# Performance work log

Hardware: AMD Instinct MI355X
Metric: run time of the kernel (lower is better)

## Reference

```python
import jax, jax.numpy as jnp
import numpy as np

B, F_DIM, P, C, H = 16, 256, 8192, 96, 256


def setup_inputs() -> dict:
    key = jax.random.key(0)
    ks = jax.random.split(key, 8)
    seg_feat = jax.random.normal(ks[0], (B, F_DIM, P), dtype=jnp.float32)
    seg_label = jax.random.randint(ks[1], (B, P), 0, C, dtype=jnp.int64 if jax.config.read('jax_enable_x64') else jnp.int32)
    s1 = 1.0 / np.sqrt(F_DIM)
    s2 = 1.0 / np.sqrt(H)
    w1 = jax.random.uniform(ks[2], (F_DIM, H), jnp.float32, -s1, s1)
    b1 = jax.random.uniform(ks[3], (H,), jnp.float32, -s1, s1)
    w2 = jax.random.uniform(ks[4], (H, H), jnp.float32, -s2, s2)
    b2 = jax.random.uniform(ks[5], (H,), jnp.float32, -s2, s2)
    w_logit = jax.random.uniform(ks[6], (H, C), jnp.float32, -s2, s2)
    b_logit = jax.random.uniform(ks[7], (C,), jnp.float32, -s2, s2)
    return dict(seg_feat=seg_feat, seg_label=seg_label, w1=w1, b1=b1,
                w2=w2, b2=b2, w_logit=w_logit, b_logit=b_logit)


def _pool_by_class(seg_feat, seg_label, num_classes):
    # seg_feat: [B, F, P], seg_label: [B, P] -> pooled [B*C, F]
    b, f, p = seg_feat.shape
    seg_ids = (jnp.arange(b, dtype=seg_label.dtype)[:, None] * num_classes
               + seg_label).reshape(-1)                       # [B*P]
    feat = seg_feat.transpose(0, 2, 1).reshape(b * p, f)      # [B*P, F]
    segmax = jax.ops.segment_max(feat, seg_ids, num_segments=b * num_classes)
    counts = jax.ops.segment_sum(jnp.ones((b * p,), feat.dtype), seg_ids,
                                 num_segments=b * num_classes)  # [B*C]
    counts = counts[:, None]
    # torch: max over points of feat * onehot -> zeros from other classes
    # participate in the max unless the class covers ALL points; empty
    # classes pool to 0 (max of all zeros).
    pooled = jnp.where(counts == 0, 0.0,
                       jnp.where(counts == p, segmax, jnp.maximum(segmax, 0.0)))
    return pooled


def reference(seg_feat, seg_label, w1, b1, w2, b2, w_logit, b_logit):
    num_classes = w_logit.shape[1]
    pooled = _pool_by_class(seg_feat, seg_label, num_classes)   # [B*C, F]
    # feat_mlp: Linear+ReLU x2 (dropout_prob=0), then part_logit
    h = jax.nn.relu(pooled @ w1 + b1)
    h = jax.nn.relu(h @ w2 + b2)
    part_pred = h @ w_logit + b_logit                           # [B*C, C]
    b = seg_feat.shape[0]
    part_batch = jnp.repeat(jnp.arange(b), num_classes)
    part_label = jnp.tile(jnp.arange(num_classes), b)
    return part_pred, part_label, part_batch
```

## Files before the change

### kernel.cpp

```cpp
#include <hip/hip_runtime.h>

#define B 16
#define F_DIM 256
#define P 8192
#define C 96
#define H 256
#define NSEG (B * C)
#define G 8
#define NFBLK (F_DIM / G)
#define SPLIT 4
#define PQ (P / SPLIT)


__global__ __launch_bounds__(256) void pool_kernel(const float* __restrict__ feat,
                                                   const int* __restrict__ label,
                                                   int* __restrict__ kbuf,
                                                   int* __restrict__ cnts) {
    __shared__ int smax[G][C];
    __shared__ int hist[C];
    const int blk = blockIdx.x;
    const int q  = blk & 3;
    const int fg = (blk >> 2) & 31;
    const int b  = blk >> 7;
    const int f0 = fg << 3;
    const int t = threadIdx.x;

    for (int i = t; i < G * C; i += 256) ((int*)smax)[i] = 0x80000000;
    if (t < C) hist[t] = 0;
    __syncthreads();

    const int4* lrow4 = (const int4*)(label + (size_t)b * P + (size_t)q * PQ);
    int4 lab[2];
    lab[0] = lrow4[t];
    lab[1] = lrow4[t + 256];

    if (fg == 0) {
        #pragma unroll
        for (int j = 0; j < 2; ++j) {
            atomicAdd(&hist[lab[j].x], 1);
            atomicAdd(&hist[lab[j].y], 1);
            atomicAdd(&hist[lab[j].z], 1);
            atomicAdd(&hist[lab[j].w], 1);
        }
    }

    const float4* fbase4 = (const float4*)(feat + ((size_t)b * F_DIM + f0) * P + (size_t)q * PQ);

    float4 cur[2], nxt[2];
    cur[0] = fbase4[t];
    cur[1] = fbase4[t + 256];

    #pragma unroll
    for (int f = 0; f < G; ++f) {
        if (f + 1 < G) {
            nxt[0] = fbase4[(size_t)(f + 1) * (P / 4) + t];
            nxt[1] = fbase4[(size_t)(f + 1) * (P / 4) + t + 256];
        }
        #pragma unroll
        for (int j = 0; j < 2; ++j) {
            atomicMax(&smax[f][lab[j].x], __float_as_int(cur[j].x));
            atomicMax(&smax[f][lab[j].y], __float_as_int(cur[j].y));
            atomicMax(&smax[f][lab[j].z], __float_as_int(cur[j].z));
            atomicMax(&smax[f][lab[j].w], __float_as_int(cur[j].w));
        }
        cur[0] = nxt[0];
        cur[1] = nxt[1];
    }
    __syncthreads();

    if (fg == 0 && t < C) cnts[q * NSEG + b * C + t] = hist[t];

    if (t < C) {
        int4 lo, hi;
        lo.x = smax[0][t]; lo.y = smax[1][t]; lo.z = smax[2][t]; lo.w = smax[3][t];
        hi.x = smax[4][t]; hi.y = smax[5][t]; hi.z = smax[6][t]; hi.w = smax[7][t];
        int* dst = kbuf + (size_t)q * NSEG * F_DIM + (size_t)(b * C + t) * F_DIM + f0;
        *(int4*)dst = lo;
        *(int4*)(dst + 4) = hi;
    }
}

template <int COLS, int RELU, int OUTW, int POOLIN>
__global__ __launch_bounds__(256, 3) void dense_kernel(const float* __restrict__ x,
                                                       const int* __restrict__ kx,
                                                       const int* __restrict__ cnts,
                                                       const float* __restrict__ w,
                                                       const float* __restrict__ bias,
                                                       float* __restrict__ y,
                                                       float* __restrict__ tails) {
    constexpr int NQ = COLS / 4;
    __shared__ float xs[8][H];
    __shared__ float ps[8][COLS][17];
    const int t = threadIdx.x;
    const int row0 = blockIdx.x * 8;
    const int bj0 = blockIdx.y * COLS;

    if (POOLIN) {
        const int4* k4 = (const int4*)kx;
        const size_t base = (size_t)row0 * (H / 4);
        #pragma unroll
        for (int jj = 0; jj < 2; ++jj) {
            const int i = t + jj * 256;
            int4 km = k4[base + i];
            #pragma unroll
            for (int h = 1; h < SPLIT; ++h) {
                const int4 kh = k4[(size_t)h * NSEG * (H / 4) + base + i];
                km.x = km.x > kh.x ? km.x : kh.x;
                km.y = km.y > kh.y ? km.y : kh.y;
                km.z = km.z > kh.z ? km.z : kh.z;
                km.w = km.w > kh.w ? km.w : kh.w;
            }
            const int row = row0 + (i >> 6);
            const int cnt = cnts[row] + cnts[NSEG + row] +
                            cnts[2 * NSEG + row] + cnts[3 * NSEG + row];
            float4 v;
            v.x = __int_as_float(km.x); v.y = __int_as_float(km.y);
            v.z = __int_as_float(km.z); v.w = __int_as_float(km.w);
            if (cnt == 0) {
                v.x = v.y = v.z = v.w = 0.0f;
            } else if (cnt != P) {
                v.x = fmaxf(v.x, 0.0f); v.y = fmaxf(v.y, 0.0f);
                v.z = fmaxf(v.z, 0.0f); v.w = fmaxf(v.w, 0.0f);
            }
            ((float4*)xs)[i] = v;
        }
    } else {
        int i0 = t, i1 = t + 256;
        ((float4*)xs)[i0] = ((const float4*)(x + (size_t)row0 * H))[i0];
        ((float4*)xs)[i1] = ((const float4*)(x + (size_t)row0 * H))[i1];
    }
    __syncthreads();

    const int s = t >> 4;
    const int jq = t & 15;

    if (jq < NQ) {
        const float4* w4 = (const float4*)w;
        constexpr int WS4 = OUTW / 4;
        const int wq = (bj0 >> 2) + jq;
        const int kbase = s * 16;
        float4 acc[8];
        #pragma unroll
        for (int r = 0; r < 8; ++r) acc[r] = (float4){0.f, 0.f, 0.f, 0.f};

        #pragma unroll
        for (int i = 0; i < 16; ++i) {
            const int k = kbase + i;
            const float4 wv = w4[k * WS4 + wq];
            #pragma unroll
            for (int r = 0; r < 8; ++r) {
                const float xv = xs[r][k];
                acc[r].x = fmaf(xv, wv.x, acc[r].x);
                acc[r].y = fmaf(xv, wv.y, acc[r].y);
                acc[r].z = fmaf(xv, wv.z, acc[r].z);
                acc[r].w = fmaf(xv, wv.w, acc[r].w);
            }
        }
        #pragma unroll
        for (int r = 0; r < 8; ++r) {
            ps[r][jq * 4 + 0][s] = acc[r].x;
            ps[r][jq * 4 + 1][s] = acc[r].y;
            ps[r][jq * 4 + 2][s] = acc[r].z;
            ps[r][jq * 4 + 3][s] = acc[r].w;
        }
    }
    __syncthreads();

    for (int e = t; e < 8 * COLS; e += 256) {
        const int r = e / COLS, j = e % COLS;
        float v = bias[bj0 + j];
        #pragma unroll
        for (int q = 0; q < 16; ++q) v += ps[r][j][q];
        if (RELU) v = fmaxf(v, 0.0f);
        y[(size_t)(row0 + r) * OUTW + bj0 + j] = v;
    }

    if (tails != nullptr && t < 8) {
        const int row = row0 + t;
        tails[row] = (float)(row % C);
        tails[NSEG + row] = (float)(row / C);
    }
}

extern "C" void kernel_launch(void* const* d_in, const int* in_sizes, int n_in,
                              void* d_out, int out_size, void* d_ws, size_t ws_size,
                              hipStream_t stream) {
    const float* feat  = (const float*)d_in[0];
    const int*   label = (const int*)d_in[1];
    const float* w1    = (const float*)d_in[2];
    const float* b1    = (const float*)d_in[3];
    const float* w2    = (const float*)d_in[4];
    const float* b2    = (const float*)d_in[5];
    const float* wl    = (const float*)d_in[6];
    const float* bl    = (const float*)d_in[7];
    float* out = (float*)d_out;

    char* ws = (char*)d_ws;
    const size_t KBYTES = (size_t)SPLIT * NSEG * H * 4;
    int*   kbuf = (int*)ws;
    int*   cnts = (int*)(ws + KBYTES);
    float* h1   = (float*)(ws + KBYTES + 32768);
    float* h2   = (float*)(ws + KBYTES + 32768 + (size_t)NSEG * H * 4);

    pool_kernel<<<B * NFBLK * SPLIT, 256, 0, stream>>>(feat, label, kbuf, cnts);
    dense_kernel<64, 1, H, 1><<<dim3(NSEG / 8, 4), 256, 0, stream>>>(nullptr, kbuf, cnts, w1, b1, h1, nullptr);
    dense_kernel<64, 1, H, 0><<<dim3(NSEG / 8, 4), 256, 0, stream>>>(h1, nullptr, nullptr, w2, b2, h2, nullptr);
    dense_kernel<48, 0, C, 0><<<dim3(NSEG / 8, 2), 256, 0, stream>>>(h2, nullptr, nullptr, wl, bl, out, out + (size_t)NSEG * C);
}
```

Measured before the change: 44.40 us.

## Fuse second hidden layer and logit layer into one kernel

Replaces the two separate dense launches for layer 2 and the logit layer with a single kernel in which each block computes all 256 hidden columns for 8 rows, keeps the ReLU output in shared memory, and then computes the 96 logits from it. This drops one kernel launch and the global round trip of the h2 intermediate. In exchange each block does more serial work (64-step k-loop per thread) and uses more shared memory, and the grid shrinks to 192 blocks, which lowers parallelism on a large GPU.

```diff
diff --git a/kernel.cpp b/kernel.cpp
--- a/kernel.cpp
+++ b/kernel.cpp
@@ -80,22 +80,19 @@
     }
 }
 
-template <int COLS, int RELU, int OUTW, int POOLIN>
-__global__ __launch_bounds__(256, 3) void dense_kernel(const float* __restrict__ x,
-                                                       const int* __restrict__ kx,
-                                                       const int* __restrict__ cnts,
-                                                       const float* __restrict__ w,
-                                                       const float* __restrict__ bias,
-                                                       float* __restrict__ y,
-                                                       float* __restrict__ tails) {
-    constexpr int NQ = COLS / 4;
+__global__ __launch_bounds__(256, 3) void dense1_kernel(const int* __restrict__ kx,
+                                                        const int* __restrict__ cnts,
+                                                        const float* __restrict__ w,
+                                                        const float* __restrict__ bias,
+                                                        float* __restrict__ y) {
+    constexpr int COLS = 64;
     __shared__ float xs[8][H];
     __shared__ float ps[8][COLS][17];
     const int t = threadIdx.x;
     const int row0 = blockIdx.x * 8;
     const int bj0 = blockIdx.y * COLS;
 
-    if (POOLIN) {
+    {
         const int4* k4 = (const int4*)kx;
         const size_t base = (size_t)row0 * (H / 4);
         #pragma unroll
@@ -124,19 +121,14 @@
             }
             ((float4*)xs)[i] = v;
         }
-    } else {
-        int i0 = t, i1 = t + 256;
-        ((float4*)xs)[i0] = ((const float4*)(x + (size_t)row0 * H))[i0];
-        ((float4*)xs)[i1] = ((const float4*)(x + (size_t)row0 * H))[i1];
     }
     __syncthreads();
 
     const int s = t >> 4;
     const int jq = t & 15;
 
-    if (jq < NQ) {
+    {
         const float4* w4 = (const float4*)w;
-        constexpr int WS4 = OUTW / 4;
         const int wq = (bj0 >> 2) + jq;
         const int kbase = s * 16;
         float4 acc[8];
@@ -146,7 +138,7 @@
         #pragma unroll
         for (int i = 0; i < 16; ++i) {
             const int k = kbase + i;
-            const float4 wv = w4[k * WS4 + wq];
+            const float4 wv = w4[k * (H / 4) + wq];
             #pragma unroll
             for (int r = 0; r < 8; ++r) {
                 const float xv = xs[r][k];
@@ -170,12 +162,94 @@
         const int r = e / COLS, j = e % COLS;
         float v = bias[bj0 + j];
         #pragma unroll
-        for (int q = 0; q < 16; ++q) v += ps[r][j][q];
-        if (RELU) v = fmaxf(v, 0.0f);
-        y[(size_t)(row0 + r) * OUTW + bj0 + j] = v;
-    }
-
-    if (tails != nullptr && t < 8) {
+        for (int qq = 0; qq < 16; ++qq) v += ps[r][j][qq];
+        y[(size_t)(row0 + r) * H + bj0 + j] = fmaxf(v, 0.0f);
+    }
+}
+
+__global__ __launch_bounds__(256, 2) void dense23_kernel(const float* __restrict__ h1,
+                                                         const float* __restrict__ w2,
+                                                         const float* __restrict__ b2,
+                                                         const float* __restrict__ wl,
+                                                         const float* __restrict__ bl,
+                                                         float* __restrict__ out,
+                                                         float* __restrict__ tails) {
+    __shared__ float xs[8][H];
+    __shared__ float xs2[8][H];
+    __shared__ float ps[8][H][5];
+    float (*ps2)[C][3] = (float(*)[C][3])ps;
+    const int t = threadIdx.x;
+    const int row0 = blockIdx.x * 8;
+
+    ((float4*)xs)[t]       = ((const float4*)(h1 + (size_t)row0 * H))[t];
+    ((float4*)xs)[t + 256] = ((const float4*)(h1 + (size_t)row0 * H))[t + 256];
+    __syncthreads();
+
+    {
+        const int jq = t & 63;
+        const int s  = t >> 6;
+        const float4* w4 = (const float4*)w2;
+        const int kbase = s * 64;
+        float4 acc[8];
+        #pragma unroll
+        for (int r = 0; r < 8; ++r) acc[r] = (float4){0.f, 0.f, 0.f, 0.f};
+
+        #pragma unroll 8
+        for (int i = 0; i < 64; ++i) {
+            const int k = kbase + i;
+            const float4 wv = w4[k * (H / 4) + jq];
+            #pragma unroll
+            for (int r = 0; r < 8; ++r) {
+                const float xv = xs[r][k];
+                acc[r].x = fmaf(xv, wv.x, acc[r].x);
+                acc[r].y = fmaf(xv, wv.y, acc[r].y);
+                acc[r].z = fmaf(xv, wv.z, acc[r].z);
+                acc[r].w = fmaf(xv, wv.w, acc[r].w);
+            }
+        }
+        #pragma unroll
+        for (int r = 0; r < 8; ++r) {
+            ps[r][jq * 4 + 0][s] = acc[r].x;
+            ps[r][jq * 4 + 1][s] = acc[r].y;
+            ps[r][jq * 4 + 2][s] = acc[r].z;
+            ps[r][jq * 4 + 3][s] = acc[r].w;
+        }
+    }
+    __syncthreads();
+
+    #pragma unroll
+    for (int e = t; e < 8 * H; e += 256) {
+        const int r = e >> 8, j = e & 255;
+        float v = b2[j] + ps[r][j][0] + ps[r][j][1] + ps[r][j][2] + ps[r][j][3];
+        xs2[r][j] = fmaxf(v, 0.0f);
+    }
+    __syncthreads();
+
+    if (t < 192) {
+        const int half = t / C;
+        const int j = t - half * C;
+        const int kbase = half * 128;
+        float acc[8];
+        #pragma unroll
+        for (int r = 0; r < 8; ++r) acc[r] = 0.0f;
+        #pragma unroll 8
+        for (int i = 0; i < 128; ++i) {
+            const int k = kbase + i;
+            const float wv = wl[k * C + j];
+            #pragma unroll
+            for (int r = 0; r < 8; ++r) acc[r] = fmaf(xs2[r][k], wv, acc[r]);
+        }
+        #pragma unroll
+        for (int r = 0; r < 8; ++r) ps2[r][j][half] = acc[r];
+    }
+    __syncthreads();
+
+    for (int e = t; e < 8 * C; e += 256) {
+        const int r = e / C, j = e % C;
+        out[(size_t)(row0 + r) * C + j] = bl[j] + ps2[r][j][0] + ps2[r][j][1];
+    }
+
+    if (t < 8) {
         const int row = row0 + t;
         tails[row] = (float)(row % C);
         tails[NSEG + row] = (float)(row / C);
@@ -200,10 +274,8 @@
     int*   kbuf = (int*)ws;
     int*   cnts = (int*)(ws + KBYTES);
     float* h1   = (float*)(ws + KBYTES + 32768);
-    float* h2   = (float*)(ws + KBYTES + 32768 + (size_t)NSEG * H * 4);
 
     pool_kernel<<<B * NFBLK * SPLIT, 256, 0, stream>>>(feat, label, kbuf, cnts);
-    dense_kernel<64, 1, H, 1><<<dim3(NSEG / 8, 4), 256, 0, stream>>>(nullptr, kbuf, cnts, w1, b1, h1, nullptr);
-    dense_kernel<64, 1, H, 0><<<dim3(NSEG / 8, 4), 256, 0, stream>>>(h1, nullptr, nullptr, w2, b2, h2, nullptr);
-    dense_kernel<48, 0, C, 0><<<dim3(NSEG / 8, 2), 256, 0, stream>>>(h2, nullptr, nullptr, wl, bl, out, out + (size_t)NSEG * C);
-}
+    dense1_kernel<<<dim3(NSEG / 8, 4), 256, 0, stream>>>(kbuf, cnts, w1, b1, h1);
+    dense23_kernel<<<NSEG / 8, 256, 0, stream>>>(h1, w2, b2, wl, bl, out, out + (size_t)NSEG * C);
+}
```

Result: slower. 48.60 us (+9.4%).
